# Kernel optimization log

Hardware: AMD Instinct MI355X
Metric: run time of the kernel (lower is better)

Reference implementation:

```python
import jax, jax.numpy as jnp
import numpy as np
from jax import lax

B = 16384
ENC_LEN = 48
ENC_HID = 128   # 2 * enc_dim (bidirectional)
DEC_DIM = 32
IN_DIM = 4
T_DEC = 12


def setup_inputs() -> dict:
    key = jax.random.key(0)
    ks = jax.random.split(key, 12)
    f32 = jnp.float32
    return {
        "y": jax.random.normal(ks[0], (B, 13, IN_DIM), f32),
        "encoder_outputs": jax.random.normal(ks[1], (ENC_LEN, B, ENC_HID), f32),
        "hidden": jax.random.normal(ks[2], (B, DEC_DIM), f32),
        "batch_ids": jax.random.randint(ks[3], (B,), 0, 1000),
        "attn_W": jax.random.normal(ks[4], (ENC_LEN, IN_DIM + DEC_DIM), f32) * 0.1,
        "attn_b": jnp.zeros((ENC_LEN,), f32),
        "comb_W": jax.random.normal(ks[5], (IN_DIM, IN_DIM + ENC_HID), f32) * 0.1,
        "comb_b": jnp.zeros((IN_DIM,), f32),
        "w_ih": jax.random.normal(ks[6], (3 * DEC_DIM, IN_DIM), f32) * 0.1,
        "w_hh": jax.random.normal(ks[7], (3 * DEC_DIM, DEC_DIM), f32) * 0.1,
        "b_ih": jnp.zeros((3 * DEC_DIM,), f32),
        "b_hh": jnp.zeros((3 * DEC_DIM,), f32),
        "fc_W": jax.random.normal(ks[8], (1, DEC_DIM), f32) * 0.1,
        "fc_b": jnp.zeros((1,), f32),
    }


def _gru_cell(x, h, w_ih, w_hh, b_ih, b_hh):
    # torch GRU gate ordering: r, z, n
    gi = x @ w_ih.T + b_ih          # (B, 3*DEC_DIM)
    gh = h @ w_hh.T + b_hh
    i_r, i_z, i_n = jnp.split(gi, 3, axis=1)
    h_r, h_z, h_n = jnp.split(gh, 3, axis=1)
    r = jax.nn.sigmoid(i_r + h_r)
    z = jax.nn.sigmoid(i_z + h_z)
    n = jnp.tanh(i_n + r * h_n)
    return (1.0 - z) * n + z * h


def reference(y, encoder_outputs, hidden, batch_ids, attn_W, attn_b,
              comb_W, comb_b, w_ih, w_hh, b_ih, b_hh, fc_W, fc_b):
    # y: (B, 13, 4) -> y_: (13, B, 4); encoder_outputs: (ENC_LEN, B, 128) -> (B, ENC_LEN, 128)
    y_ = jnp.transpose(y, (1, 0, 2))
    enc = jnp.transpose(encoder_outputs, (1, 0, 2))
    x0 = jnp.nan_to_num(y_[0])  # rnn_input[rnn_input != rnn_input] = 0
    # dropout(p=0.5) treated as identity (eval mode)

    def step(carry, y_next3):
        x, h = carry  # x: (B, IN_DIM), h: (B, DEC_DIM)
        # Bahdanau-ish attention: softmax over enc_len positions
        attn_logits = jnp.concatenate([x, h], axis=1) @ attn_W.T + attn_b  # (B, ENC_LEN)
        aw = jax.nn.softmax(attn_logits, axis=1)
        ctx = jnp.einsum('be,bed->bd', aw, enc)  # (B, ENC_HID)
        x2 = jnp.concatenate([ctx, x], axis=1) @ comb_W.T + comb_b  # (B, IN_DIM)
        h = _gru_cell(x2, h, w_ih, w_hh, b_ih, b_hh)
        out = h @ fc_W.T + fc_b  # (B, 1)
        x_next = jnp.concatenate([y_next3, out], axis=1)  # (B, IN_DIM)
        return (x_next, h), out

    xs = y_[1:13, :, 1:]  # (12, B, 3): next-step exogenous features
    (_, _), outs = lax.scan(step, (x0, hidden), xs)  # outs: (12, B, 1)
    y_pred = outs[:, :, 0]  # cat(dim=1).transpose(0,1) -> (12, B)
    return y_pred
```

## Files before the change

### kernel.cpp

```cpp
#include <hip/hip_runtime.h>

#define B 16384
#define ENC_LEN 48
#define ENC_HID 128
#define T_DEC 12

#define NWAVE 16
#define EPW 3
#define UPW 2

__device__ __forceinline__ float fast_rcp(float x) { return __builtin_amdgcn_rcpf(x); }
__device__ __forceinline__ float fast_exp(float x) { return __expf(x); }
__device__ __forceinline__ float sigmoidf_(float x) { return fast_rcp(1.f + fast_exp(-x)); }
__device__ __forceinline__ float tanhf_(float x) {
    return 1.f - 2.f * fast_rcp(1.f + fast_exp(2.f * x));
}
__device__ __forceinline__ float nan_to_num_(float v) { return (v != v) ? 0.f : v; }

__global__ __launch_bounds__(256) void precompute_P_kernel(
    const float* __restrict__ enc,
    const float* __restrict__ cW,
    float4* __restrict__ P)
{
    const int l = threadIdx.x & 7;
    const int rowLocal = threadIdx.x >> 3;

    float w[4][4][4];
    #pragma unroll
    for (int i = 0; i < 4; ++i)
        #pragma unroll
        for (int k = 0; k < 4; ++k) {
            float4 t = *(const float4*)(cW + i * 132 + k * 32 + l * 4);
            w[i][k][0] = t.x; w[i][k][1] = t.y; w[i][k][2] = t.z; w[i][k][3] = t.w;
        }

    const int totalRows = ENC_LEN * B;
    const int stride = gridDim.x * 32;
    for (int row = blockIdx.x * 32 + rowLocal; row < totalRows; row += stride) {
        const float* r = enc + (size_t)row * ENC_HID;
        float4 e[4];
        #pragma unroll
        for (int k = 0; k < 4; ++k)
            e[k] = *(const float4*)(r + k * 32 + l * 4);

        float a[4];
        #pragma unroll
        for (int i = 0; i < 4; ++i) {
            float s0 = e[0].x * w[i][0][0] + e[0].y * w[i][0][1] + e[0].z * w[i][0][2] + e[0].w * w[i][0][3];
            float s1 = e[1].x * w[i][1][0] + e[1].y * w[i][1][1] + e[1].z * w[i][1][2] + e[1].w * w[i][1][3];
            float s2 = e[2].x * w[i][2][0] + e[2].y * w[i][2][1] + e[2].z * w[i][2][2] + e[2].w * w[i][2][3];
            float s3 = e[3].x * w[i][3][0] + e[3].y * w[i][3][1] + e[3].z * w[i][3][2] + e[3].w * w[i][3][3];
            a[i] = (s0 + s1) + (s2 + s3);
        }
        #pragma unroll
        for (int m = 1; m < 8; m <<= 1) {
            #pragma unroll
            for (int i = 0; i < 4; ++i)
                a[i] += __shfl_xor(a[i], m, 8);
        }
        if (l == 0) P[row] = make_float4(a[0], a[1], a[2], a[3]);
    }
}

__global__ __launch_bounds__(1024, 4) void decode_kernel(
    const float* __restrict__ y,
    const float* __restrict__ hidden,
    const float4* __restrict__ P,
    const float* __restrict__ aW,
    const float* __restrict__ ab,
    const float* __restrict__ cW,
    const float* __restrict__ cb,
    const float* __restrict__ wih,
    const float* __restrict__ whh,
    const float* __restrict__ bih,
    const float* __restrict__ bhh,
    const float* __restrict__ fW,
    const float* __restrict__ fb,
    float* __restrict__ out)
{
    __shared__ float sh_h[64 * 36];
    __shared__ float sh_red[2][64][6];

    const int lane = threadIdx.x & 63;
    const int w = __builtin_amdgcn_readfirstlane(threadIdx.x >> 6);
    const int b = blockIdx.x * 64 + lane;

    {
        float2 v = *(const float2*)(hidden + (size_t)b * 32 + w * 2);
        *(float2*)(&sh_h[lane * 36 + w * 2]) = v;
    }
    for (int i = threadIdx.x; i < 2 * 64 * 6; i += 1024)
        (&sh_red[0][0][0])[i] = 0.f;

    float4 pb[EPW];
    #pragma unroll
    for (int i = 0; i < EPW; ++i)
        pb[i] = P[(size_t)(w * EPW + i) * B + b];

    float xA[4];
    #pragma unroll
    for (int k = 0; k < 4; ++k)
        xA[k] = nan_to_num_(y[(size_t)b * 52 + k]);

    __syncthreads();

    for (int t = 0; t < T_DEC; ++t) {
        const int buf = t & 1;

        float h[32];
        #pragma unroll
        for (int k = 0; k < 8; ++k) {
            float4 v = *(const float4*)(&sh_h[lane * 36 + k * 4]);
            h[k * 4 + 0] = v.x; h[k * 4 + 1] = v.y; h[k * 4 + 2] = v.z; h[k * 4 + 3] = v.w;
        }

        float Sp = 0.f, c0 = 0.f, c1 = 0.f, c2 = 0.f, c3 = 0.f;
        #pragma unroll
        for (int i = 0; i < EPW; ++i) {
            const int e = w * EPW + i;
            const float* wr = aW + e * 36;
            float s = ab[e] + wr[0] * xA[0] + wr[1] * xA[1] + wr[2] * xA[2] + wr[3] * xA[3];
            #pragma unroll
            for (int j = 0; j < 32; ++j) s += wr[4 + j] * h[j];
            float g = fast_exp(s);
            Sp += g;
            c0 += g * pb[i].x; c1 += g * pb[i].y; c2 += g * pb[i].z; c3 += g * pb[i].w;
        }
        atomicAdd(&sh_red[buf][lane][0], Sp);
        atomicAdd(&sh_red[buf][lane][1], c0);
        atomicAdd(&sh_red[buf][lane][2], c1);
        atomicAdd(&sh_red[buf][lane][3], c2);
        atomicAdd(&sh_red[buf][lane][4], c3);

        __syncthreads();

        const float S  = sh_red[buf][lane][0];
        const float rs = fast_rcp(S);
        float x2g[4];
        #pragma unroll
        for (int i = 0; i < 4; ++i) {
            const float* cr = cW + i * 132 + 128;
            x2g[i] = sh_red[buf][lane][1 + i] * rs
                   + cr[0] * xA[0] + cr[1] * xA[1] + cr[2] * xA[2] + cr[3] * xA[3] + cb[i];
        }
        if (w == 0) {
            #pragma unroll
            for (int k = 0; k < 6; ++k) sh_red[buf ^ 1][lane][k] = 0.f;
        }

        float hn[UPW];
        #pragma unroll
        for (int u = 0; u < UPW; ++u) {
            const int g = w * UPW + u;
            float ir = bih[g], iz = bih[g + 32], in_ = bih[g + 64];
            #pragma unroll
            for (int k = 0; k < 4; ++k) {
                ir  += wih[g * 4 + k]        * x2g[k];
                iz  += wih[(g + 32) * 4 + k] * x2g[k];
                in_ += wih[(g + 64) * 4 + k] * x2g[k];
            }
            float hr = bhh[g], hz = bhh[g + 32], hn_ = bhh[g + 64];
            #pragma unroll
            for (int k = 0; k < 32; ++k) {
                hr  += whh[g * 32 + k]        * h[k];
                hz  += whh[(g + 32) * 32 + k] * h[k];
                hn_ += whh[(g + 64) * 32 + k] * h[k];
            }
            float r = sigmoidf_(ir + hr);
            float z = sigmoidf_(iz + hz);
            float n = tanhf_(in_ + r * hn_);
            hn[u] = (1.f - z) * n + z * h[g];
        }
        *(float2*)(&sh_h[lane * 36 + w * UPW]) = make_float2(hn[0], hn[1]);

        atomicAdd(&sh_red[buf][lane][5], fW[w * UPW] * hn[0] + fW[w * UPW + 1] * hn[1]);

        __syncthreads();

        const float o = sh_red[buf][lane][5] + fb[0];
        if (w == 0) out[t * B + b] = o;

        if (t < T_DEC - 1) {
            float4 yv = *(const float4*)(y + (size_t)b * 52 + (t + 1) * 4);
            xA[0] = yv.y; xA[1] = yv.z; xA[2] = yv.w; xA[3] = o;
        }
    }
}

extern "C" void kernel_launch(void* const* d_in, const int* in_sizes, int n_in,
                              void* d_out, int out_size, void* d_ws, size_t ws_size,
                              hipStream_t stream)
{
    const float* y   = (const float*)d_in[0];
    const float* enc = (const float*)d_in[1];
    const float* hid = (const float*)d_in[2];
    const float* aW  = (const float*)d_in[4];
    const float* ab  = (const float*)d_in[5];
    const float* cW  = (const float*)d_in[6];
    const float* cb  = (const float*)d_in[7];
    const float* wih = (const float*)d_in[8];
    const float* whh = (const float*)d_in[9];
    const float* bih = (const float*)d_in[10];
    const float* bhh = (const float*)d_in[11];
    const float* fW  = (const float*)d_in[12];
    const float* fb  = (const float*)d_in[13];
    float* out = (float*)d_out;

    float4* P = (float4*)d_ws;

    precompute_P_kernel<<<4096, 256, 0, stream>>>(enc, cW, P);
    decode_kernel<<<B / 64, 1024, 0, stream>>>(
        y, hid, P, aW, ab, cW, cb, wih, whh, bih, bhh, fW, fb, out);
}
```

Baseline: 698.7 us.

## Remap decode to 16 lanes per batch row with wave-level shuffle reductions

Restructures the decode kernel so each batch element is handled by 16 lanes within one wave, not 16 waves sharing LDS. Cross-wave reductions done with shared-memory atomics and block barriers become xor-shuffle reductions inside the wave, and the hidden-state broadcast uses ds_bpermute. All weights are staged once into LDS as float4 rows, so each timestep avoids scalar global reads. The cost is more lanes per element doing shuffle work and a different occupancy profile, while the precompute kernel, which likely dominates total time, is unchanged.

```diff
diff --git a/kernel.cpp b/kernel.cpp
--- a/kernel.cpp
+++ b/kernel.cpp
@@ -4,10 +4,6 @@
 #define ENC_LEN 48
 #define ENC_HID 128
 #define T_DEC 12
-
-#define NWAVE 16
-#define EPW 3
-#define UPW 2
 
 __device__ __forceinline__ float fast_rcp(float x) { return __builtin_amdgcn_rcpf(x); }
 __device__ __forceinline__ float fast_exp(float x) { return __expf(x); }
@@ -16,6 +12,9 @@
     return 1.f - 2.f * fast_rcp(1.f + fast_exp(2.f * x));
 }
 __device__ __forceinline__ float nan_to_num_(float v) { return (v != v) ? 0.f : v; }
+__device__ __forceinline__ float bperm(int byteidx, float v) {
+    return __int_as_float(__builtin_amdgcn_ds_bpermute(byteidx, __float_as_int(v)));
+}
 
 __global__ __launch_bounds__(256) void precompute_P_kernel(
     const float* __restrict__ enc,
@@ -62,7 +61,7 @@
     }
 }
 
-__global__ __launch_bounds__(1024, 4) void decode_kernel(
+__global__ __launch_bounds__(256, 4) void decode_kernel(
     const float* __restrict__ y,
     const float* __restrict__ hidden,
     const float4* __restrict__ P,
@@ -78,112 +77,129 @@
     const float* __restrict__ fb,
     float* __restrict__ out)
 {
-    __shared__ float sh_h[64 * 36];
-    __shared__ float sh_red[2][64][6];
-
-    const int lane = threadIdx.x & 63;
-    const int w = __builtin_amdgcn_readfirstlane(threadIdx.x >> 6);
-    const int b = blockIdx.x * 64 + lane;
-
-    {
-        float2 v = *(const float2*)(hidden + (size_t)b * 32 + w * 2);
-        *(float2*)(&sh_h[lane * 36 + w * 2]) = v;
-    }
-    for (int i = threadIdx.x; i < 2 * 64 * 6; i += 1024)
-        (&sh_red[0][0][0])[i] = 0.f;
-
-    float4 pb[EPW];
-    #pragma unroll
-    for (int i = 0; i < EPW; ++i)
-        pb[i] = P[(size_t)(w * EPW + i) * B + b];
-
-    float xA[4];
-    #pragma unroll
-    for (int k = 0; k < 4; ++k)
-        xA[k] = nan_to_num_(y[(size_t)b * 52 + k]);
+    __shared__ __align__(16) float aW_l[48 * 36];
+    __shared__ __align__(16) float whh_l[96 * 36];
+    __shared__ __align__(16) float wih_l[96 * 4];
+    __shared__ float bih_l[96], bhh_l[96], ab_l[48], fW_l[32], cWt_l[16], cb_l[4];
+
+    const int tid = threadIdx.x;
+
+    for (int i = tid; i < 48 * 36; i += 256) aW_l[i] = aW[i];
+    for (int i = tid; i < 96 * 32; i += 256) whh_l[(i >> 5) * 36 + (i & 31)] = whh[i];
+    for (int i = tid; i < 96 * 4; i += 256) wih_l[i] = wih[i];
+    if (tid < 96) { bih_l[tid] = bih[tid]; bhh_l[tid] = bhh[tid]; }
+    if (tid < 48) ab_l[tid] = ab[tid];
+    if (tid < 32) fW_l[tid] = fW[tid];
+    if (tid < 16) cWt_l[tid] = cW[(tid >> 2) * 132 + 128 + (tid & 3)];
+    if (tid < 4)  cb_l[tid] = cb[tid];
+
+    const int lane  = tid & 63;
+    const int q     = lane & 15;
+    const int b     = blockIdx.x * 16 + (tid >> 4);
+    const int pbase = (lane & 48) << 2;
+
+    float4 pb0 = P[(size_t)(3 * q + 0) * B + b];
+    float4 pb1 = P[(size_t)(3 * q + 1) * B + b];
+    float4 pb2 = P[(size_t)(3 * q + 2) * B + b];
+
+    float h0 = hidden[(size_t)b * 32 + q];
+    float h1 = hidden[(size_t)b * 32 + q + 16];
+
+    float xA0 = nan_to_num_(y[(size_t)b * 52 + 0]);
+    float xA1 = nan_to_num_(y[(size_t)b * 52 + 1]);
+    float xA2 = nan_to_num_(y[(size_t)b * 52 + 2]);
+    float xA3 = nan_to_num_(y[(size_t)b * 52 + 3]);
 
     __syncthreads();
 
+    const float fb0 = fb[0];
+
+    #pragma unroll 1
     for (int t = 0; t < T_DEC; ++t) {
-        const int buf = t & 1;
-
-        float h[32];
-        #pragma unroll
-        for (int k = 0; k < 8; ++k) {
-            float4 v = *(const float4*)(&sh_h[lane * 36 + k * 4]);
-            h[k * 4 + 0] = v.x; h[k * 4 + 1] = v.y; h[k * 4 + 2] = v.z; h[k * 4 + 3] = v.w;
-        }
+        float4 yv = make_float4(0.f, 0.f, 0.f, 0.f);
+        if (t < T_DEC - 1) yv = *(const float4*)(y + (size_t)b * 52 + (t + 1) * 4);
+
+        float hf[32];
+        #pragma unroll
+        for (int j = 0; j < 16; ++j) hf[j] = bperm(pbase + (j << 2), h0);
+        #pragma unroll
+        for (int j = 0; j < 16; ++j) hf[16 + j] = bperm(pbase + (j << 2), h1);
 
         float Sp = 0.f, c0 = 0.f, c1 = 0.f, c2 = 0.f, c3 = 0.f;
         #pragma unroll
-        for (int i = 0; i < EPW; ++i) {
-            const int e = w * EPW + i;
-            const float* wr = aW + e * 36;
-            float s = ab[e] + wr[0] * xA[0] + wr[1] * xA[1] + wr[2] * xA[2] + wr[3] * xA[3];
-            #pragma unroll
-            for (int j = 0; j < 32; ++j) s += wr[4 + j] * h[j];
+        for (int i = 0; i < 3; ++i) {
+            const int e = 3 * q + i;
+            const float4* wr = (const float4*)(aW_l + e * 36);
+            float4 w0 = wr[0];
+            float s = ab_l[e] + w0.x * xA0 + w0.y * xA1 + w0.z * xA2 + w0.w * xA3;
+            #pragma unroll
+            for (int c = 0; c < 8; ++c) {
+                float4 wc = wr[1 + c];
+                s += wc.x * hf[4 * c] + wc.y * hf[4 * c + 1]
+                   + wc.z * hf[4 * c + 2] + wc.w * hf[4 * c + 3];
+            }
             float g = fast_exp(s);
             Sp += g;
-            c0 += g * pb[i].x; c1 += g * pb[i].y; c2 += g * pb[i].z; c3 += g * pb[i].w;
-        }
-        atomicAdd(&sh_red[buf][lane][0], Sp);
-        atomicAdd(&sh_red[buf][lane][1], c0);
-        atomicAdd(&sh_red[buf][lane][2], c1);
-        atomicAdd(&sh_red[buf][lane][3], c2);
-        atomicAdd(&sh_red[buf][lane][4], c3);
-
-        __syncthreads();
-
-        const float S  = sh_red[buf][lane][0];
-        const float rs = fast_rcp(S);
-        float x2g[4];
-        #pragma unroll
-        for (int i = 0; i < 4; ++i) {
-            const float* cr = cW + i * 132 + 128;
-            x2g[i] = sh_red[buf][lane][1 + i] * rs
-                   + cr[0] * xA[0] + cr[1] * xA[1] + cr[2] * xA[2] + cr[3] * xA[3] + cb[i];
-        }
-        if (w == 0) {
-            #pragma unroll
-            for (int k = 0; k < 6; ++k) sh_red[buf ^ 1][lane][k] = 0.f;
-        }
-
-        float hn[UPW];
-        #pragma unroll
-        for (int u = 0; u < UPW; ++u) {
-            const int g = w * UPW + u;
-            float ir = bih[g], iz = bih[g + 32], in_ = bih[g + 64];
-            #pragma unroll
-            for (int k = 0; k < 4; ++k) {
-                ir  += wih[g * 4 + k]        * x2g[k];
-                iz  += wih[(g + 32) * 4 + k] * x2g[k];
-                in_ += wih[(g + 64) * 4 + k] * x2g[k];
+            float4 pbv = (i == 0) ? pb0 : ((i == 1) ? pb1 : pb2);
+            c0 += g * pbv.x; c1 += g * pbv.y; c2 += g * pbv.z; c3 += g * pbv.w;
+        }
+        #pragma unroll
+        for (int m = 1; m < 16; m <<= 1) {
+            Sp += __shfl_xor(Sp, m);
+            c0 += __shfl_xor(c0, m);
+            c1 += __shfl_xor(c1, m);
+            c2 += __shfl_xor(c2, m);
+            c3 += __shfl_xor(c3, m);
+        }
+        const float rs = fast_rcp(Sp);
+
+        float x2[4];
+        {
+            float cc[4] = { c0, c1, c2, c3 };
+            #pragma unroll
+            for (int i = 0; i < 4; ++i)
+                x2[i] = cc[i] * rs
+                      + cWt_l[i * 4 + 0] * xA0 + cWt_l[i * 4 + 1] * xA1
+                      + cWt_l[i * 4 + 2] * xA2 + cWt_l[i * 4 + 3] * xA3 + cb_l[i];
+        }
+
+        float hn0, hn1;
+        #pragma unroll
+        for (int u = 0; u < 2; ++u) {
+            const int g = q + 16 * u;
+            const float hu = (u == 0) ? h0 : h1;
+            const float4* w4r = (const float4*)(whh_l + (size_t)g * 36);
+            const float4* w4z = (const float4*)(whh_l + (size_t)(g + 32) * 36);
+            const float4* w4n = (const float4*)(whh_l + (size_t)(g + 64) * 36);
+            float hr = bhh_l[g], hz = bhh_l[g + 32], hn_ = bhh_l[g + 64];
+            #pragma unroll
+            for (int c = 0; c < 8; ++c) {
+                float4 a = w4r[c], bz = w4z[c], cn = w4n[c];
+                hr  += a.x  * hf[4 * c] + a.y  * hf[4 * c + 1] + a.z  * hf[4 * c + 2] + a.w  * hf[4 * c + 3];
+                hz  += bz.x * hf[4 * c] + bz.y * hf[4 * c + 1] + bz.z * hf[4 * c + 2] + bz.w * hf[4 * c + 3];
+                hn_ += cn.x * hf[4 * c] + cn.y * hf[4 * c + 1] + cn.z * hf[4 * c + 2] + cn.w * hf[4 * c + 3];
             }
-            float hr = bhh[g], hz = bhh[g + 32], hn_ = bhh[g + 64];
-            #pragma unroll
-            for (int k = 0; k < 32; ++k) {
-                hr  += whh[g * 32 + k]        * h[k];
-                hz  += whh[(g + 32) * 32 + k] * h[k];
-                hn_ += whh[(g + 64) * 32 + k] * h[k];
-            }
+            const float4 wiR = *(const float4*)(wih_l + (size_t)g * 4);
+            const float4 wiZ = *(const float4*)(wih_l + (size_t)(g + 32) * 4);
+            const float4 wiN = *(const float4*)(wih_l + (size_t)(g + 64) * 4);
+            float ir  = bih_l[g]      + wiR.x * x2[0] + wiR.y * x2[1] + wiR.z * x2[2] + wiR.w * x2[3];
+            float iz  = bih_l[g + 32] + wiZ.x * x2[0] + wiZ.y * x2[1] + wiZ.z * x2[2] + wiZ.w * x2[3];
+            float in_ = bih_l[g + 64] + wiN.x * x2[0] + wiN.y * x2[1] + wiN.z * x2[2] + wiN.w * x2[3];
             float r = sigmoidf_(ir + hr);
             float z = sigmoidf_(iz + hz);
             float n = tanhf_(in_ + r * hn_);
-            hn[u] = (1.f - z) * n + z * h[g];
-        }
-        *(float2*)(&sh_h[lane * 36 + w * UPW]) = make_float2(hn[0], hn[1]);
-
-        atomicAdd(&sh_red[buf][lane][5], fW[w * UPW] * hn[0] + fW[w * UPW + 1] * hn[1]);
-
-        __syncthreads();
-
-        const float o = sh_red[buf][lane][5] + fb[0];
-        if (w == 0) out[t * B + b] = o;
-
-        if (t < T_DEC - 1) {
-            float4 yv = *(const float4*)(y + (size_t)b * 52 + (t + 1) * 4);
-            xA[0] = yv.y; xA[1] = yv.z; xA[2] = yv.w; xA[3] = o;
-        }
+            float hnv = (1.f - z) * n + z * hu;
+            if (u == 0) hn0 = hnv; else hn1 = hnv;
+        }
+
+        float op = fW_l[q] * hn0 + fW_l[q + 16] * hn1;
+        #pragma unroll
+        for (int m = 1; m < 16; m <<= 1) op += __shfl_xor(op, m);
+        const float o = op + fb0;
+        if (q == 0) out[(size_t)t * B + b] = o;
+
+        h0 = hn0; h1 = hn1;
+        if (t < T_DEC - 1) { xA0 = yv.y; xA1 = yv.z; xA2 = yv.w; xA3 = o; }
     }
 }
 
@@ -209,6 +225,6 @@
     float4* P = (float4*)d_ws;
 
     precompute_P_kernel<<<4096, 256, 0, stream>>>(enc, cW, P);
-    decode_kernel<<<B / 64, 1024, 0, stream>>>(
+    decode_kernel<<<B / 16, 256, 0, stream>>>(
         y, hid, P, aW, ab, cW, cb, wih, whh, bih, bhh, fW, fb, out);
 }
```

Result: slower. 1.189 ms (+70.2%).
